# Performance work log

Measured on AMD Instinct MI355X. Metric: run time of the kernel, lower is better.

The kernel has to match this reference:

```python
import jax, jax.numpy as jnp
import numpy as np

NU, NI, D, LAYERS, NNZ = 50000, 50000, 256, 2, 400000
N = NU + NI
LEAKY_ALPHA = 0.2  # tf.nn.leaky_relu default


def setup_inputs() -> dict:
    key = jax.random.key(0)
    ks = jax.random.split(key, 32)
    inp = {}
    inp["initial_ebs"] = jax.random.normal(ks[0], (N, D), jnp.float32) * 0.1
    for i, nm in enumerate(["W_side_u", "W_dot_u", "W_side_i", "W_dot_i"]):
        inp[nm] = jax.random.normal(ks[1 + i], (LAYERS, D, D), jnp.float32) / np.float32(np.sqrt(D))
    vi = 5
    for ent, ne in (("u", NU), ("i", NI)):
        for mat in ("LI", "L"):
            inp[f"{mat}_vals_{ent}"] = jax.random.uniform(ks[vi], (NNZ,), jnp.float32); vi += 1
            inp[f"{mat}_rows_{ent}"] = jnp.sort(jax.random.randint(ks[vi], (NNZ,), 0, ne, jnp.int32)); vi += 1
            inp[f"{mat}_cols_{ent}"] = jax.random.randint(ks[vi], (NNZ,), 0, N, jnp.int32); vi += 1
    return inp


def _spmm(rows, cols, vals, ebs, n_rows):
    # sparse [n_rows, N] @ dense [N, D] via gather + segment-sum
    return jax.ops.segment_sum(vals[:, None] * ebs[cols], rows, num_segments=n_rows)


def reference(initial_ebs, W_side_u, W_dot_u, W_side_i, W_dot_i,
              LI_vals_u, L_vals_u, LI_vals_i, L_vals_i,
              LI_rows_u, LI_cols_u, L_rows_u, L_cols_u,
              LI_rows_i, LI_cols_i, L_rows_i, L_cols_i):
    ebs = initial_ebs
    layers_ebs = []
    for l in range(LAYERS):
        # entity 'u': rows [0, NU)
        li_u = _spmm(LI_rows_u, LI_cols_u, LI_vals_u, ebs, NU)
        l_u = _spmm(L_rows_u, L_cols_u, L_vals_u, ebs, NU)
        fold_u = jax.nn.leaky_relu(li_u @ W_side_u[l] + (l_u * ebs[:NU]) @ W_dot_u[l], LEAKY_ALPHA)
        # entity 'i': rows [NU, N)
        li_i = _spmm(LI_rows_i, LI_cols_i, LI_vals_i, ebs, NI)
        l_i = _spmm(L_rows_i, L_cols_i, L_vals_i, ebs, NI)
        fold_i = jax.nn.leaky_relu(li_i @ W_side_i[l] + (l_i * ebs[NU:]) @ W_dot_i[l], LEAKY_ALPHA)
        ebs = jnp.concatenate([fold_u, fold_i], axis=0)  # [N, D]
        layers_ebs.append(ebs)
    return jnp.concatenate(layers_ebs, axis=0)  # [LAYERS*N, D]
```

## Files before the change

### kernel.cpp

```cpp
#include <hip/hip_runtime.h>

#define NUQ 50000
#define NIQ 50000
#define DQ 256
#define NTOT 100000
#define LALPHA 0.2f

typedef __attribute__((ext_vector_type(8))) __bf16 bf16x8;
typedef __attribute__((ext_vector_type(4))) float floatx4;

__device__ __forceinline__ float b2f(unsigned short u) {
    unsigned int x = ((unsigned int)u) << 16;
    return __builtin_bit_cast(float, x);
}
__device__ __forceinline__ unsigned short f2b(float f) {
    unsigned int u = __builtin_bit_cast(unsigned int, f);
    u = u + 0x7FFFu + ((u >> 16) & 1u);
    return (unsigned short)(u >> 16);
}

#define GLD_LDS16(g, l)                                                        \
    __builtin_amdgcn_global_load_lds(                                          \
        (const __attribute__((address_space(1))) void*)(g),                    \
        (__attribute__((address_space(3))) void*)(l), 16, 0, 0)

__global__ __launch_bounds__(256) void build_rowptr(
    const int* __restrict__ rows, int nnz, int* __restrict__ rptr, int n_rows)
{
    int e = blockIdx.x * 256 + threadIdx.x;
    if (e > nnz) return;
    int prev = (e == 0)   ? -1     : rows[e - 1];
    int cur  = (e == nnz) ? n_rows : rows[e];
    for (int r = prev + 1; r <= cur; ++r) rptr[r] = e;
}

__global__ __launch_bounds__(256) void cvt_f32_bf16(
    const float* __restrict__ in, unsigned short* __restrict__ out, int n4)
{
    int i = blockIdx.x * 256 + threadIdx.x;
    if (i >= n4) return;
    float4 v = ((const float4*)in)[i];
    ushort4 o;
    o.x = f2b(v.x); o.y = f2b(v.y); o.z = f2b(v.z); o.w = f2b(v.w);
    ((ushort4*)out)[i] = o;
}

__global__ __launch_bounds__(256) void build_bt(
    const float* __restrict__ Ws_u, const float* __restrict__ Wd_u,
    const float* __restrict__ Ws_i, const float* __restrict__ Wd_i,
    unsigned short* __restrict__ Bt)
{
    int idx = blockIdx.x * 256 + threadIdx.x;
    int k   = idx & 511;
    int n   = (idx >> 9) & 255;
    int buf = idx >> 17;
    int l = buf >> 1, e = buf & 1;
    const float* Wside = e ? Ws_i : Ws_u;
    const float* Wdot  = e ? Wd_i : Wd_u;
    float v = (k < 256) ? Wside[((size_t)l * 256 + k)       * 256 + n]
                        : Wdot [((size_t)l * 256 + (k-256)) * 256 + n];
    Bt[idx] = f2b(v);
}

__global__ __launch_bounds__(256) void spmm_dual_bf16(
    const int* __restrict__ rptrA, const int* __restrict__ colsA, const float* __restrict__ valsA,
    const int* __restrict__ rptrB, const int* __restrict__ colsB, const float* __restrict__ valsB,
    const unsigned short* __restrict__ src,
    const unsigned short* __restrict__ mul,
    unsigned short* __restrict__ out,
    int n_rows)
{
    const int wave = threadIdx.x >> 6;
    const int lane = threadIdx.x & 63;
    const int row  = blockIdx.x * 4 + wave;
    if (row >= n_rows) return;
    const bool isB = (blockIdx.y != 0);

    const int*   rptr = isB ? rptrB : rptrA;
    const int*   cols = isB ? colsB : colsA;
    const float* vals = isB ? valsB : valsA;

    const int start = rptr[row];
    const int end   = rptr[row + 1];

    ushort4 mraw = {0, 0, 0, 0};
    if (isB) mraw = ((const ushort4*)(mul + (size_t)row * DQ))[lane];

    float ax = 0.f, ay = 0.f, az = 0.f, aw = 0.f;
    int e = start;
    for (; e + 4 <= end; e += 4) {
        int   c0 = cols[e],     c1 = cols[e + 1], c2 = cols[e + 2], c3 = cols[e + 3];
        float v0 = vals[e],     v1 = vals[e + 1], v2 = vals[e + 2], v3 = vals[e + 3];
        ushort4 s0 = ((const ushort4*)(src + (size_t)c0 * DQ))[lane];
        ushort4 s1 = ((const ushort4*)(src + (size_t)c1 * DQ))[lane];
        ushort4 s2 = ((const ushort4*)(src + (size_t)c2 * DQ))[lane];
        ushort4 s3 = ((const ushort4*)(src + (size_t)c3 * DQ))[lane];
        ax = fmaf(v0, b2f(s0.x), ax); ay = fmaf(v0, b2f(s0.y), ay);
        az = fmaf(v0, b2f(s0.z), az); aw = fmaf(v0, b2f(s0.w), aw);
        ax = fmaf(v1, b2f(s1.x), ax); ay = fmaf(v1, b2f(s1.y), ay);
        az = fmaf(v1, b2f(s1.z), az); aw = fmaf(v1, b2f(s1.w), aw);
        ax = fmaf(v2, b2f(s2.x), ax); ay = fmaf(v2, b2f(s2.y), ay);
        az = fmaf(v2, b2f(s2.z), az); aw = fmaf(v2, b2f(s2.w), aw);
        ax = fmaf(v3, b2f(s3.x), ax); ay = fmaf(v3, b2f(s3.y), ay);
        az = fmaf(v3, b2f(s3.z), az); aw = fmaf(v3, b2f(s3.w), aw);
    }
    for (; e < end; ++e) {
        int   c = cols[e];
        float v = vals[e];
        ushort4 s = ((const ushort4*)(src + (size_t)c * DQ))[lane];
        ax = fmaf(v, b2f(s.x), ax); ay = fmaf(v, b2f(s.y), ay);
        az = fmaf(v, b2f(s.z), az); aw = fmaf(v, b2f(s.w), aw);
    }
    if (isB) {
        ax *= b2f(mraw.x); ay *= b2f(mraw.y);
        az *= b2f(mraw.z); aw *= b2f(mraw.w);
    }
    ushort4 o;
    o.x = f2b(ax); o.y = f2b(ay); o.z = f2b(az); o.w = f2b(aw);
    ((ushort4*)(out + (size_t)row * 512 + (isB ? 256 : 0)))[lane] = o;
}

__global__ __launch_bounds__(256) void gemm_mfma_leaky(
    const unsigned short* __restrict__ A,
    const unsigned short* __restrict__ Bt,
    float* __restrict__ out,
    int M)
{
    __shared__ unsigned short As[4096];
    __shared__ unsigned short Bs[4096];

    const int tid  = threadIdx.x;
    const int lane = tid & 63;
    const int w    = tid >> 6;
    const int row0 = blockIdx.x * 128;
    const int n0   = blockIdx.y * 128;

    const int m_off = (w & 1) * 64;
    const int n_off = (w >> 1) * 64;

    floatx4 acc[4][4] = {};

    const unsigned short* gA[2];
    const unsigned short* gB[2];
    int ldsoff[2];
    #pragma unroll
    for (int j = 0; j < 2; ++j) {
        int c = w * 2 + j;
        int t = c * 64 + lane;
        int m    = ((t >> 6) << 4) | (t & 15);
        int kblk = (t >> 4) & 3;
        int gr = row0 + m; if (gr >= M) gr = M - 1;
        gA[j] = A  + (size_t)gr * 512 + kblk * 8;
        gB[j] = Bt + (size_t)(n0 + m) * 512 + kblk * 8;
        ldsoff[j] = c * 512;
    }

    const int lr = lane >> 4;
    const int lc = lane & 15;

    for (int kt = 0; kt < 16; ++kt) {
        const int k0 = kt * 32;
        #pragma unroll
        for (int j = 0; j < 2; ++j) {
            GLD_LDS16(gA[j] + k0, &As[ldsoff[j]]);
            GLD_LDS16(gB[j] + k0, &Bs[ldsoff[j]]);
        }
        __syncthreads();

        bf16x8 af[4], bfr[4];
        #pragma unroll
        for (int tm = 0; tm < 4; ++tm)
            af[tm] = *(const bf16x8*)&As[((m_off >> 4) + tm) * 512 + lr * 128 + lc * 8];
        #pragma unroll
        for (int tn = 0; tn < 4; ++tn)
            bfr[tn] = *(const bf16x8*)&Bs[((n_off >> 4) + tn) * 512 + lr * 128 + lc * 8];

        #pragma unroll
        for (int tm = 0; tm < 4; ++tm)
            #pragma unroll
            for (int tn = 0; tn < 4; ++tn)
                acc[tm][tn] = __builtin_amdgcn_mfma_f32_16x16x32_bf16(
                    af[tm], bfr[tn], acc[tm][tn], 0, 0, 0);

        __syncthreads();
    }

    #pragma unroll
    for (int tm = 0; tm < 4; ++tm) {
        #pragma unroll
        for (int r = 0; r < 4; ++r) {
            int gr = row0 + m_off + tm * 16 + lr * 4 + r;
            if (gr >= M) continue;
            float* orow = out + (size_t)gr * 256;
            #pragma unroll
            for (int tn = 0; tn < 4; ++tn) {
                int gc = n0 + n_off + tn * 16 + lc;
                float v = acc[tm][tn][r];
                orow[gc] = v > 0.f ? v : LALPHA * v;
            }
        }
    }
}

extern "C" void kernel_launch(void* const* d_in, const int* in_sizes, int n_in,
                              void* d_out, int out_size, void* d_ws, size_t ws_size,
                              hipStream_t stream) {
    const float* ebs0      = (const float*)d_in[0];
    const float* W_side_u  = (const float*)d_in[1];
    const float* W_dot_u   = (const float*)d_in[2];
    const float* W_side_i  = (const float*)d_in[3];
    const float* W_dot_i   = (const float*)d_in[4];
    const float* LI_vals_u = (const float*)d_in[5];
    const int*   LI_rows_u = (const int*)  d_in[6];
    const int*   LI_cols_u = (const int*)  d_in[7];
    const float* L_vals_u  = (const float*)d_in[8];
    const int*   L_rows_u  = (const int*)  d_in[9];
    const int*   L_cols_u  = (const int*)  d_in[10];
    const float* LI_vals_i = (const float*)d_in[11];
    const int*   LI_rows_i = (const int*)  d_in[12];
    const int*   LI_cols_i = (const int*)  d_in[13];
    const float* L_vals_i  = (const float*)d_in[14];
    const int*   L_rows_i  = (const int*)  d_in[15];
    const int*   L_cols_i  = (const int*)  d_in[16];

    float* out = (float*)d_out;

    unsigned short* Abuf   = (unsigned short*)d_ws;
    unsigned short* ebs_bf = (unsigned short*)((char*)d_ws + 51200000);
    unsigned short* Bt     = (unsigned short*)((char*)d_ws + 102400000);
    int* rp_LI_u = (int*)((char*)d_ws + 103448576);
    int* rp_L_u  = rp_LI_u + 50001;
    int* rp_LI_i = rp_L_u  + 50001;
    int* rp_L_i  = rp_LI_i + 50001;

    const int nnz_LI_u = in_sizes[5];
    const int nnz_L_u  = in_sizes[8];
    const int nnz_LI_i = in_sizes[11];
    const int nnz_L_i  = in_sizes[14];

    dim3 b256(256);
    build_rowptr<<<dim3((nnz_LI_u + 256) / 256), b256, 0, stream>>>(LI_rows_u, nnz_LI_u, rp_LI_u, NUQ);
    build_rowptr<<<dim3((nnz_L_u  + 256) / 256), b256, 0, stream>>>(L_rows_u,  nnz_L_u,  rp_L_u,  NUQ);
    build_rowptr<<<dim3((nnz_LI_i + 256) / 256), b256, 0, stream>>>(LI_rows_i, nnz_LI_i, rp_LI_i, NIQ);
    build_rowptr<<<dim3((nnz_L_i  + 256) / 256), b256, 0, stream>>>(L_rows_i,  nnz_L_i,  rp_L_i,  NIQ);
    build_bt<<<dim3(2048), b256, 0, stream>>>(W_side_u, W_dot_u, W_side_i, W_dot_i, Bt);
    cvt_f32_bf16<<<dim3(25000), b256, 0, stream>>>(ebs0, ebs_bf, NTOT * DQ / 4);

    dim3 sgrid((NUQ + 3) / 4, 2);
    dim3 ggrid((NUQ + 127) / 128, 2);

    for (int l = 0; l < 2; ++l) {
        float* outl = out + (size_t)l * NTOT * DQ;

        spmm_dual_bf16<<<sgrid, b256, 0, stream>>>(rp_LI_u, LI_cols_u, LI_vals_u,
                                                   rp_L_u,  L_cols_u,  L_vals_u,
                                                   ebs_bf, ebs_bf, Abuf, NUQ);
        gemm_mfma_leaky<<<ggrid, b256, 0, stream>>>(Abuf, Bt + (size_t)(l * 2 + 0) * 131072,
                                                    outl, NUQ);
        spmm_dual_bf16<<<sgrid, b256, 0, stream>>>(rp_LI_i, LI_cols_i, LI_vals_i,
                                                   rp_L_i,  L_cols_i,  L_vals_i,
                                                   ebs_bf, ebs_bf + (size_t)NUQ * DQ, Abuf, NIQ);
        gemm_mfma_leaky<<<ggrid, b256, 0, stream>>>(Abuf, Bt + (size_t)(l * 2 + 1) * 131072,
                                                    outl + (size_t)NUQ * DQ, NIQ);

        if (l == 0)
            cvt_f32_bf16<<<dim3(25000), b256, 0, stream>>>(outl, ebs_bf, NTOT * DQ / 4);
    }
}
```

Baseline: 769.2 us.

## Merge entity SpMM/GEMM launches, double-buffer GEMM, fuse bf16 writeback

The user and item SpMMs now run in a single launch over all rows, and so do their GEMMs. Each SpMM wave loads its column indices and values cooperatively, shuffles them to lanes, and has each half-wave gather 16-byte row segments before a cross-half reduction. The GEMM switches to 64x256 tiles with double-buffered LDS prefetch, and during layer 0 it writes bf16 activations directly from its epilogue, which removes the separate conversion pass. Abuf is sized for both entities, so the workspace grows.

```diff
diff --git a/kernel.cpp b/kernel.cpp
--- a/kernel.cpp
+++ b/kernel.cpp
@@ -5,9 +5,11 @@
 #define DQ 256
 #define NTOT 100000
 #define LALPHA 0.2f
+#define GPE 782
 
 typedef __attribute__((ext_vector_type(8))) __bf16 bf16x8;
 typedef __attribute__((ext_vector_type(4))) float floatx4;
+typedef __attribute__((ext_vector_type(8))) unsigned short ushort8;
 
 __device__ __forceinline__ float b2f(unsigned short u) {
     unsigned int x = ((unsigned int)u) << 16;
@@ -62,141 +64,158 @@
     Bt[idx] = f2b(v);
 }
 
-__global__ __launch_bounds__(256) void spmm_dual_bf16(
-    const int* __restrict__ rptrA, const int* __restrict__ colsA, const float* __restrict__ valsA,
-    const int* __restrict__ rptrB, const int* __restrict__ colsB, const float* __restrict__ valsB,
+__global__ __launch_bounds__(256) void spmm_dual_v2(
+    const int* __restrict__ rpA_u, const int* __restrict__ cA_u, const float* __restrict__ vA_u,
+    const int* __restrict__ rpB_u, const int* __restrict__ cB_u, const float* __restrict__ vB_u,
+    const int* __restrict__ rpA_i, const int* __restrict__ cA_i, const float* __restrict__ vA_i,
+    const int* __restrict__ rpB_i, const int* __restrict__ cB_i, const float* __restrict__ vB_i,
     const unsigned short* __restrict__ src,
-    const unsigned short* __restrict__ mul,
-    unsigned short* __restrict__ out,
-    int n_rows)
+    unsigned short* __restrict__ out)
 {
     const int wave = threadIdx.x >> 6;
     const int lane = threadIdx.x & 63;
-    const int row  = blockIdx.x * 4 + wave;
-    if (row >= n_rows) return;
-    const bool isB = (blockIdx.y != 0);
-
-    const int*   rptr = isB ? rptrB : rptrA;
-    const int*   cols = isB ? colsB : colsA;
-    const float* vals = isB ? valsB : valsA;
+    const int r    = blockIdx.x * 4 + wave;
+    if (r >= NTOT) return;
+    const int  isB = blockIdx.y;
+    const bool isI = (r >= NUQ);
+    const int  row = isI ? (r - NUQ) : r;
+
+    const int* rptr; const int* cols; const float* vals;
+    if (isB) { rptr = isI ? rpB_i : rpB_u; cols = isI ? cB_i : cB_u; vals = isI ? vB_i : vB_u; }
+    else     { rptr = isI ? rpA_i : rpA_u; cols = isI ? cA_i : cA_u; vals = isI ? vA_i : vA_u; }
 
     const int start = rptr[row];
     const int end   = rptr[row + 1];
 
-    ushort4 mraw = {0, 0, 0, 0};
-    if (isB) mraw = ((const ushort4*)(mul + (size_t)row * DQ))[lane];
-
-    float ax = 0.f, ay = 0.f, az = 0.f, aw = 0.f;
-    int e = start;
-    for (; e + 4 <= end; e += 4) {
-        int   c0 = cols[e],     c1 = cols[e + 1], c2 = cols[e + 2], c3 = cols[e + 3];
-        float v0 = vals[e],     v1 = vals[e + 1], v2 = vals[e + 2], v3 = vals[e + 3];
-        ushort4 s0 = ((const ushort4*)(src + (size_t)c0 * DQ))[lane];
-        ushort4 s1 = ((const ushort4*)(src + (size_t)c1 * DQ))[lane];
-        ushort4 s2 = ((const ushort4*)(src + (size_t)c2 * DQ))[lane];
-        ushort4 s3 = ((const ushort4*)(src + (size_t)c3 * DQ))[lane];
-        ax = fmaf(v0, b2f(s0.x), ax); ay = fmaf(v0, b2f(s0.y), ay);
-        az = fmaf(v0, b2f(s0.z), az); aw = fmaf(v0, b2f(s0.w), aw);
-        ax = fmaf(v1, b2f(s1.x), ax); ay = fmaf(v1, b2f(s1.y), ay);
-        az = fmaf(v1, b2f(s1.z), az); aw = fmaf(v1, b2f(s1.w), aw);
-        ax = fmaf(v2, b2f(s2.x), ax); ay = fmaf(v2, b2f(s2.y), ay);
-        az = fmaf(v2, b2f(s2.z), az); aw = fmaf(v2, b2f(s2.w), aw);
-        ax = fmaf(v3, b2f(s3.x), ax); ay = fmaf(v3, b2f(s3.y), ay);
-        az = fmaf(v3, b2f(s3.z), az); aw = fmaf(v3, b2f(s3.w), aw);
-    }
-    for (; e < end; ++e) {
-        int   c = cols[e];
-        float v = vals[e];
-        ushort4 s = ((const ushort4*)(src + (size_t)c * DQ))[lane];
-        ax = fmaf(v, b2f(s.x), ax); ay = fmaf(v, b2f(s.y), ay);
-        az = fmaf(v, b2f(s.z), az); aw = fmaf(v, b2f(s.w), aw);
-    }
-    if (isB) {
-        ax *= b2f(mraw.x); ay *= b2f(mraw.y);
-        az *= b2f(mraw.z); aw *= b2f(mraw.w);
-    }
-    ushort4 o;
-    o.x = f2b(ax); o.y = f2b(ay); o.z = f2b(az); o.w = f2b(aw);
-    ((ushort4*)(out + (size_t)row * 512 + (isB ? 256 : 0)))[lane] = o;
-}
-
-__global__ __launch_bounds__(256) void gemm_mfma_leaky(
+    const int half = lane >> 5;
+    const int li   = lane & 31;
+
+    float acc[8] = {0.f, 0.f, 0.f, 0.f, 0.f, 0.f, 0.f, 0.f};
+
+    for (int base = start; base < end; base += 64) {
+        int cnt = end - base; if (cnt > 64) cnt = 64;
+        int myc = 0; float myv = 0.f;
+        if (lane < cnt) { myc = cols[base + lane]; myv = vals[base + lane]; }
+        #pragma unroll 2
+        for (int e = 0; e < cnt; e += 2) {
+            const int idx = e + half;
+            const int   c = __shfl(myc, idx, 64);
+            const float v = __shfl(myv, idx, 64);
+            const ushort8 s = *(const ushort8*)(src + (size_t)c * DQ + li * 8);
+            #pragma unroll
+            for (int j = 0; j < 8; ++j) acc[j] = fmaf(v, b2f(s[j]), acc[j]);
+        }
+    }
+
+    #pragma unroll
+    for (int j = 0; j < 8; ++j) acc[j] += __shfl_xor(acc[j], 32, 64);
+
+    if (half == 0) {
+        if (isB) {
+            const ushort8 m = *(const ushort8*)(src + (size_t)r * DQ + li * 8);
+            #pragma unroll
+            for (int j = 0; j < 8; ++j) acc[j] *= b2f(m[j]);
+        }
+        ushort8 o;
+        #pragma unroll
+        for (int j = 0; j < 8; ++j) o[j] = f2b(acc[j]);
+        *(ushort8*)(out + (size_t)r * 512 + isB * 256 + li * 8) = o;
+    }
+}
+
+__global__ __launch_bounds__(256) void gemm_mfma_leaky_v2(
     const unsigned short* __restrict__ A,
-    const unsigned short* __restrict__ Bt,
+    const unsigned short* __restrict__ Btl,
     float* __restrict__ out,
-    int M)
-{
-    __shared__ unsigned short As[4096];
-    __shared__ unsigned short Bs[4096];
+    unsigned short* __restrict__ ebs,
+    const int wb)
+{
+    __shared__ unsigned short As[2][2048];
+    __shared__ unsigned short Bs[2][8192];
 
     const int tid  = threadIdx.x;
     const int lane = tid & 63;
     const int w    = tid >> 6;
-    const int row0 = blockIdx.x * 128;
-    const int n0   = blockIdx.y * 128;
-
-    const int m_off = (w & 1) * 64;
-    const int n_off = (w >> 1) * 64;
-
-    floatx4 acc[4][4] = {};
-
-    const unsigned short* gA[2];
-    const unsigned short* gB[2];
-    int ldsoff[2];
-    #pragma unroll
-    for (int j = 0; j < 2; ++j) {
-        int c = w * 2 + j;
-        int t = c * 64 + lane;
-        int m    = ((t >> 6) << 4) | (t & 15);
-        int kblk = (t >> 4) & 3;
-        int gr = row0 + m; if (gr >= M) gr = M - 1;
-        gA[j] = A  + (size_t)gr * 512 + kblk * 8;
-        gB[j] = Bt + (size_t)(n0 + m) * 512 + kblk * 8;
-        ldsoff[j] = c * 512;
-    }
-
-    const int lr = lane >> 4;
-    const int lc = lane & 15;
-
+    const int ent  = (blockIdx.x >= GPE) ? 1 : 0;
+    const int bx   = blockIdx.x - ent * GPE;
+    const int row0 = ent * NUQ + bx * 64;
+    const int Mend = ent * NUQ + NUQ;
+    const unsigned short* Bt = Btl + (size_t)ent * 131072;
+
+    const int mA  = ((tid >> 6) << 4) | (tid & 15);
+    const int kbA = (tid >> 4) & 3;
+    int grs = row0 + mA; if (grs >= Mend) grs = Mend - 1;
+    const unsigned short* gA = A + (size_t)grs * 512 + kbA * 8;
+    const int ldsA = w * 512;
+
+    const unsigned short* gB[4];
+    #pragma unroll
+    for (int j = 0; j < 4; ++j) {
+        int t = j * 256 + tid;
+        int n = ((t >> 6) << 4) | (t & 15);
+        gB[j] = Bt + (size_t)n * 512 + ((t >> 4) & 3) * 8;
+    }
+    const int ldsB = w * 512;
+
+    const int lr  = lane >> 4;
+    const int lc  = lane & 15;
+    const int gmb = (w & 1) * 2;
+    const int gnb = (w >> 1) * 8;
+
+    floatx4 acc[2][8] = {};
+
+    GLD_LDS16(gA, &As[0][ldsA]);
+    #pragma unroll
+    for (int j = 0; j < 4; ++j)
+        GLD_LDS16(gB[j], &Bs[0][j * 2048 + ldsB]);
+    __syncthreads();
+
+    int cur = 0;
     for (int kt = 0; kt < 16; ++kt) {
-        const int k0 = kt * 32;
-        #pragma unroll
-        for (int j = 0; j < 2; ++j) {
-            GLD_LDS16(gA[j] + k0, &As[ldsoff[j]]);
-            GLD_LDS16(gB[j] + k0, &Bs[ldsoff[j]]);
-        }
-        __syncthreads();
-
-        bf16x8 af[4], bfr[4];
-        #pragma unroll
-        for (int tm = 0; tm < 4; ++tm)
-            af[tm] = *(const bf16x8*)&As[((m_off >> 4) + tm) * 512 + lr * 128 + lc * 8];
-        #pragma unroll
-        for (int tn = 0; tn < 4; ++tn)
-            bfr[tn] = *(const bf16x8*)&Bs[((n_off >> 4) + tn) * 512 + lr * 128 + lc * 8];
-
-        #pragma unroll
-        for (int tm = 0; tm < 4; ++tm)
-            #pragma unroll
-            for (int tn = 0; tn < 4; ++tn)
+        if (kt < 15) {
+            const int ko = (kt + 1) * 32;
+            GLD_LDS16(gA + ko, &As[cur ^ 1][ldsA]);
+            #pragma unroll
+            for (int j = 0; j < 4; ++j)
+                GLD_LDS16(gB[j] + ko, &Bs[cur ^ 1][j * 2048 + ldsB]);
+        }
+
+        bf16x8 af[2], bfr[8];
+        #pragma unroll
+        for (int tm = 0; tm < 2; ++tm)
+            af[tm] = *(const bf16x8*)&As[cur][(gmb + tm) * 512 + lr * 128 + lc * 8];
+        #pragma unroll
+        for (int tn = 0; tn < 8; ++tn)
+            bfr[tn] = *(const bf16x8*)&Bs[cur][(gnb + tn) * 512 + lr * 128 + lc * 8];
+
+        #pragma unroll
+        for (int tm = 0; tm < 2; ++tm)
+            #pragma unroll
+            for (int tn = 0; tn < 8; ++tn)
                 acc[tm][tn] = __builtin_amdgcn_mfma_f32_16x16x32_bf16(
                     af[tm], bfr[tn], acc[tm][tn], 0, 0, 0);
 
         __syncthreads();
-    }
-
-    #pragma unroll
-    for (int tm = 0; tm < 4; ++tm) {
-        #pragma unroll
-        for (int r = 0; r < 4; ++r) {
-            int gr = row0 + m_off + tm * 16 + lr * 4 + r;
-            if (gr >= M) continue;
-            float* orow = out + (size_t)gr * 256;
-            #pragma unroll
-            for (int tn = 0; tn < 4; ++tn) {
-                int gc = n0 + n_off + tn * 16 + lc;
-                float v = acc[tm][tn][r];
-                orow[gc] = v > 0.f ? v : LALPHA * v;
+        cur ^= 1;
+    }
+
+    const int m_off = (w & 1) * 32;
+    const int n_off = (w >> 1) * 128;
+    #pragma unroll
+    for (int tm = 0; tm < 2; ++tm) {
+        #pragma unroll
+        for (int rr = 0; rr < 4; ++rr) {
+            const int gr = row0 + m_off + tm * 16 + lr * 4 + rr;
+            if (gr >= Mend) continue;
+            float*          orow = out + (size_t)gr * 256;
+            unsigned short* brow = ebs + (size_t)gr * 256;
+            #pragma unroll
+            for (int tn = 0; tn < 8; ++tn) {
+                const int gc = n_off + tn * 16 + lc;
+                float v = acc[tm][tn][rr];
+                v = v > 0.f ? v : LALPHA * v;
+                orow[gc] = v;
+                if (wb) brow[gc] = f2b(v);
             }
         }
     }
@@ -226,9 +245,9 @@
     float* out = (float*)d_out;
 
     unsigned short* Abuf   = (unsigned short*)d_ws;
-    unsigned short* ebs_bf = (unsigned short*)((char*)d_ws + 51200000);
-    unsigned short* Bt     = (unsigned short*)((char*)d_ws + 102400000);
-    int* rp_LI_u = (int*)((char*)d_ws + 103448576);
+    unsigned short* ebs_bf = (unsigned short*)((char*)d_ws + 102400000);
+    unsigned short* Bt     = (unsigned short*)((char*)d_ws + 153600000);
+    int* rp_LI_u = (int*)((char*)d_ws + 154648576);
     int* rp_L_u  = rp_LI_u + 50001;
     int* rp_LI_i = rp_L_u  + 50001;
     int* rp_L_i  = rp_LI_i + 50001;
@@ -246,24 +265,16 @@
     build_bt<<<dim3(2048), b256, 0, stream>>>(W_side_u, W_dot_u, W_side_i, W_dot_i, Bt);
     cvt_f32_bf16<<<dim3(25000), b256, 0, stream>>>(ebs0, ebs_bf, NTOT * DQ / 4);
 
-    dim3 sgrid((NUQ + 3) / 4, 2);
-    dim3 ggrid((NUQ + 127) / 128, 2);
+    dim3 sgrid(NTOT / 4, 2);
+    dim3 ggrid(2 * GPE);
 
     for (int l = 0; l < 2; ++l) {
         float* outl = out + (size_t)l * NTOT * DQ;
-
-        spmm_dual_bf16<<<sgrid, b256, 0, stream>>>(rp_LI_u, LI_cols_u, LI_vals_u,
-                                                   rp_L_u,  L_cols_u,  L_vals_u,
-                                                   ebs_bf, ebs_bf, Abuf, NUQ);
-        gemm_mfma_leaky<<<ggrid, b256, 0, stream>>>(Abuf, Bt + (size_t)(l * 2 + 0) * 131072,
-                                                    outl, NUQ);
-        spmm_dual_bf16<<<sgrid, b256, 0, stream>>>(rp_LI_i, LI_cols_i, LI_vals_i,
-                                                   rp_L_i,  L_cols_i,  L_vals_i,
-                                                   ebs_bf, ebs_bf + (size_t)NUQ * DQ, Abuf, NIQ);
-        gemm_mfma_leaky<<<ggrid, b256, 0, stream>>>(Abuf, Bt + (size_t)(l * 2 + 1) * 131072,
-                                                    outl + (size_t)NUQ * DQ, NIQ);
-
-        if (l == 0)
-            cvt_f32_bf16<<<dim3(25000), b256, 0, stream>>>(outl, ebs_bf, NTOT * DQ / 4);
-    }
-}
+        spmm_dual_v2<<<sgrid, b256, 0, stream>>>(
+            rp_LI_u, LI_cols_u, LI_vals_u, rp_L_u, L_cols_u, L_vals_u,
+            rp_LI_i, LI_cols_i, LI_vals_i, rp_L_i, L_cols_i, L_vals_i,
+            ebs_bf, Abuf);
+        gemm_mfma_leaky_v2<<<ggrid, b256, 0, stream>>>(
+            Abuf, Bt + (size_t)l * 2 * 131072, outl, ebs_bf, (l == 0) ? 1 : 0);
+    }
+}
```

Result: faster. 736.7 us (-4.2%).
